# Performance work log

Measured on AMD Instinct MI355X. Metric: run time of the kernel, lower is better.

## Reference

```python
import jax, jax.numpy as jnp
import numpy as np
from jax import lax

# Production-scale dims: batch, seq_len, tag_size (incl. START/STOP tags)
B, S, T = 512, 512, 64


def setup_inputs() -> dict:
    key = jax.random.key(0)
    k1, k2, k3, k4 = jax.random.split(key, 4)
    feats = jax.random.normal(k1, (B, S, T), dtype=jnp.float32)
    # prefix-contiguous mask (module assumes mask[:, 0] == 1 and length-style masks)
    lengths = jax.random.randint(k2, (B,), S // 2, S + 1)
    mask = jnp.arange(S)[None, :] < lengths[:, None]  # (B, S) bool
    tags = jax.random.randint(k3, (B, S), 0, T - 2)  # gold tags exclude START/STOP
    transitions = jax.random.normal(k4, (T, T), dtype=jnp.float32) * 0.1
    return {"feats": feats, "mask": mask, "tags": tags, "transitions": transitions}


def _crf_nll(feats, transitions, mask, tags):
    b, s, t = feats.shape
    START, STOP = t - 2, t - 1  # START_TAG = -2, STOP_TAG = -1

    # ---- forward (log partition), matches _calculate_PZ ----
    # partition init: scores[0][:, START, :] = feats[:,0,:] + transitions[START, :]
    init = feats[:, 0, :] + transitions[START][None, :]  # (b, t)

    feats_t = jnp.swapaxes(feats, 0, 1)  # (s, b, t)
    mask_t = jnp.swapaxes(mask, 0, 1)    # (s, b)

    def step(partition, inp):
        f_t, m_t = inp  # (b, t), (b,)
        # cur_values[b, from, to] = feats_t[b, to] + transitions[from, to] + partition[b, from]
        cur = partition[:, :, None] + transitions[None, :, :] + f_t[:, None, :]
        new_p = jax.nn.logsumexp(cur, axis=1)  # reduce over 'from' -> (b, t)
        partition = jnp.where(m_t[:, None], new_p, partition)
        return partition, None

    partition, _ = lax.scan(step, init, (feats_t[1:], mask_t[1:]))

    # final transition to STOP
    final = jax.nn.logsumexp(partition[:, :, None] + transitions[None, :, :], axis=1)
    forward_score = final[:, STOP].sum()

    # ---- gold score, matches _score_sentence ----
    prev = jnp.concatenate(
        [jnp.full((b, 1), START, dtype=tags.dtype), tags[:, :-1]], axis=1
    )  # (b, s): previous tag, START at position 0
    emit = jnp.take_along_axis(feats, tags[:, :, None], axis=2)[:, :, 0]  # (b, s)
    tg_energy = emit + transitions[prev, tags]  # (b, s)
    gold = jnp.where(mask, tg_energy, jnp.zeros((), feats.dtype)).sum()
    lengths = mask.sum(axis=1).astype(jnp.int32)  # (b,)
    end_ids = jnp.take_along_axis(tags, (lengths - 1)[:, None].astype(tags.dtype), axis=1)[:, 0]
    gold = gold + transitions[end_ids, STOP].sum()

    # average_batch = False
    return forward_score - gold


def reference(feats, mask, tags, transitions):
    return _crf_nll(feats, transitions, mask, tags)
```

## Files before the change

### kernel.cpp

```cpp
#include <hip/hip_runtime.h>

#define BB 512
#define SS 512
#define TT 64
#define START_TAG 62
#define STOP_TAG 63

#define LOG2E 1.4426950408889634f
#define LN2   0.6931471805599453f

typedef _Float16 h2 __attribute__((ext_vector_type(2)));
typedef _Float16 h8 __attribute__((ext_vector_type(8)));
typedef float    f4 __attribute__((ext_vector_type(4)));

__device__ __forceinline__ h2 pkrtz(float a, float b) {
    return __builtin_bit_cast(h2, __builtin_amdgcn_cvt_pkrtz(a, b));
}

__global__ void __launch_bounds__(128)
__attribute__((amdgpu_waves_per_eu(1, 1))) crf_main(
    const float* __restrict__ feats, const int* __restrict__ mask,
    const int* __restrict__ tags, const float* __restrict__ trans,
    float* __restrict__ out)
{
    const int b    = blockIdx.x;
    const int tid  = threadIdx.x;
    const int lane = tid & 63;

    const float* frow = feats + (size_t)b * SS * TT;
    const int*   mrow = mask + b * SS;

    __shared__ __align__(16) _Float16 febuf[8][TT];

    if (tid < 64) {
        const int g  = lane >> 4;
        const int cg = lane & 15;

        int cnt = 0;
        #pragma unroll
        for (int s = lane; s < SS; s += 64) cnt += (mrow[s] != 0);
        #pragma unroll
        for (int off = 32; off; off >>= 1) cnt += __shfl_xor(cnt, off);
        const int len = cnt;

        const int to_base   = 16 * (cg >> 2) + (cg & 3);
        const int from_base = 16 * g;
        h8 A[4][2];
        #pragma unroll
        for (int tt = 0; tt < 4; ++tt)
            #pragma unroll
            for (int kc = 0; kc < 2; ++kc)
                #pragma unroll
                for (int j = 0; j < 8; ++j)
                    A[tt][kc][j] = (_Float16)__builtin_amdgcn_exp2f(
                        trans[(from_base + 8 * kc + j) * TT
                              + (to_base + 4 * tt)] * LOG2E);

        const float offs = frow[0] + trans[START_TAG * TT + 0];
        h8 B0, B1;
        #pragma unroll
        for (int sl = 0; sl < 8; ++sl) {
            const int t0 = 16 * g + sl, t1 = t0 + 8;
            B0[sl] = (_Float16)__builtin_amdgcn_exp2f(
                (frow[t0] + trans[START_TAG * TT + t0] - offs) * LOG2E);
            B1[sl] = (_Float16)__builtin_amdgcn_exp2f(
                (frow[t1] + trans[START_TAG * TT + t1] - offs) * LOG2E);
        }
        int ksum = 0;
        const f4 Z = {0.f, 0.f, 0.f, 0.f};

        float fr[8];
        #pragma unroll
        for (int j = 0; j < 8; ++j) {
            int r = 1 + j; if (r > SS - 1) r = SS - 1;
            fr[j] = frow[(size_t)r * TT + lane];
        }
        #pragma unroll
        for (int j = 0; j < 4; ++j)
            febuf[(1 + j) & 7][lane] =
                (_Float16)__builtin_amdgcn_exp2f(fr[j] * LOG2E);

        auto step = [&](int row) {
            const _Float16* fb = &febuf[row & 7][16 * g];
            const h8 fe0 = *(const h8*)(fb);
            const h8 fe1 = *(const h8*)(fb + 8);
            f4 d0 = __builtin_amdgcn_mfma_f32_16x16x32_f16(A[0][0], B0, Z, 0, 0, 0);
            f4 d1 = __builtin_amdgcn_mfma_f32_16x16x32_f16(A[1][0], B0, Z, 0, 0, 0);
            f4 d2 = __builtin_amdgcn_mfma_f32_16x16x32_f16(A[2][0], B0, Z, 0, 0, 0);
            f4 d3 = __builtin_amdgcn_mfma_f32_16x16x32_f16(A[3][0], B0, Z, 0, 0, 0);
            d0 = __builtin_amdgcn_mfma_f32_16x16x32_f16(A[0][1], B1, d0, 0, 0, 0);
            d1 = __builtin_amdgcn_mfma_f32_16x16x32_f16(A[1][1], B1, d1, 0, 0, 0);
            d2 = __builtin_amdgcn_mfma_f32_16x16x32_f16(A[2][1], B1, d2, 0, 0, 0);
            d3 = __builtin_amdgcn_mfma_f32_16x16x32_f16(A[3][1], B1, d3, 0, 0, 0);
            const int eb = (__builtin_amdgcn_readfirstlane(
                                __float_as_int(d0[0])) >> 23) & 0xff;
            ksum += eb - 127;
            const float sc = __int_as_float((254 - eb) << 23);
            const h2 p0 = pkrtz(d0[0] * sc, d0[1] * sc);
            const h2 p1 = pkrtz(d0[2] * sc, d0[3] * sc);
            const h2 p2 = pkrtz(d1[0] * sc, d1[1] * sc);
            const h2 p3 = pkrtz(d1[2] * sc, d1[3] * sc);
            const h2 p4 = pkrtz(d2[0] * sc, d2[1] * sc);
            const h2 p5 = pkrtz(d2[2] * sc, d2[3] * sc);
            const h2 p6 = pkrtz(d3[0] * sc, d3[1] * sc);
            const h2 p7 = pkrtz(d3[2] * sc, d3[3] * sc);
            const h2 q0 = p0 * __builtin_shufflevector(fe0, fe0, 0, 1);
            const h2 q1 = p1 * __builtin_shufflevector(fe0, fe0, 2, 3);
            const h2 q2 = p2 * __builtin_shufflevector(fe0, fe0, 4, 5);
            const h2 q3 = p3 * __builtin_shufflevector(fe0, fe0, 6, 7);
            const h2 q4 = p4 * __builtin_shufflevector(fe1, fe1, 0, 1);
            const h2 q5 = p5 * __builtin_shufflevector(fe1, fe1, 2, 3);
            const h2 q6 = p6 * __builtin_shufflevector(fe1, fe1, 4, 5);
            const h2 q7 = p7 * __builtin_shufflevector(fe1, fe1, 6, 7);
            B0 = __builtin_shufflevector(
                     __builtin_shufflevector(q0, q1, 0, 1, 2, 3),
                     __builtin_shufflevector(q2, q3, 0, 1, 2, 3),
                     0, 1, 2, 3, 4, 5, 6, 7);
            B1 = __builtin_shufflevector(
                     __builtin_shufflevector(q4, q5, 0, 1, 2, 3),
                     __builtin_shufflevector(q6, q7, 0, 1, 2, 3),
                     0, 1, 2, 3, 4, 5, 6, 7);
        };

        int s = 1;
        for (; s + 3 < len; s += 4) {
            float n0, n1, n2, n3;
            {
                int r0 = s + 8, r1 = s + 9, r2 = s + 10, r3 = s + 11;
                if (r0 > SS - 1) r0 = SS - 1;
                if (r1 > SS - 1) r1 = SS - 1;
                if (r2 > SS - 1) r2 = SS - 1;
                if (r3 > SS - 1) r3 = SS - 1;
                n0 = frow[(size_t)r0 * TT + lane];
                n1 = frow[(size_t)r1 * TT + lane];
                n2 = frow[(size_t)r2 * TT + lane];
                n3 = frow[(size_t)r3 * TT + lane];
            }
            febuf[(s + 4) & 7][lane] =
                (_Float16)__builtin_amdgcn_exp2f(fr[4] * LOG2E);
            febuf[(s + 5) & 7][lane] =
                (_Float16)__builtin_amdgcn_exp2f(fr[5] * LOG2E);
            febuf[(s + 6) & 7][lane] =
                (_Float16)__builtin_amdgcn_exp2f(fr[6] * LOG2E);
            febuf[(s + 7) & 7][lane] =
                (_Float16)__builtin_amdgcn_exp2f(fr[7] * LOG2E);

            step(s); step(s + 1); step(s + 2); step(s + 3);

            #pragma unroll
            for (int j = 0; j < 4; ++j) fr[j] = fr[j + 4];
            fr[4] = n0; fr[5] = n1; fr[6] = n2; fr[7] = n3;
        }

        const int rem = len - s;
        if (rem > 0) step(s);
        if (rem > 1) step(s + 1);
        if (rem > 2) step(s + 2);

        float e = 0.f;
        #pragma unroll
        for (int sl = 0; sl < 8; ++sl) {
            const int t0 = 16 * g + sl, t1 = t0 + 8;
            e += (float)B0[sl] * __builtin_amdgcn_exp2f(
                     trans[t0 * TT + STOP_TAG] * LOG2E);
            e += (float)B1[sl] * __builtin_amdgcn_exp2f(
                     trans[t1 * TT + STOP_TAG] * LOG2E);
        }
        e += __shfl_xor(e, 16);
        e += __shfl_xor(e, 32);

        if (lane == 0)
            atomicAdd(out, offs + (float)ksum * LN2
                           + LN2 * __builtin_amdgcn_logf(e));
    } else {
        const int* trow = tags + b * SS;
        int   cnt = 0;
        float acc = 0.f;
        for (int s = lane; s < SS; s += 64) {
            if (mrow[s] != 0) {
                ++cnt;
                const int tag  = trow[s];
                const int prev = (s == 0) ? START_TAG : trow[s - 1];
                acc += frow[(size_t)s * TT + tag] + trans[prev * TT + tag];
            }
        }
        #pragma unroll
        for (int off = 32; off; off >>= 1) {
            acc += __shfl_xor(acc, off);
            cnt += __shfl_xor(cnt, off);
        }
        if (lane == 0) {
            const int end_id = trow[cnt - 1];
            atomicAdd(out, -(acc + trans[end_id * TT + STOP_TAG]));
        }
    }
}

extern "C" void kernel_launch(void* const* d_in, const int* in_sizes, int n_in,
                              void* d_out, int out_size, void* d_ws, size_t ws_size,
                              hipStream_t stream) {
    const float* feats = (const float*)d_in[0];
    const int*   mask  = (const int*)d_in[1];
    const int*   tags  = (const int*)d_in[2];
    const float* trans = (const float*)d_in[3];
    float* out = (float*)d_out;

    (void)hipMemsetAsync(out, 0, sizeof(float), stream);
    crf_main<<<BB, 128, 0, stream>>>(feats, mask, tags, trans, out);
}
```

Baseline: 186.4 us.

## Split CRF forward recurrence into forward and backward halves on two waves

```diff
diff --git a/kernel.cpp b/kernel.cpp
--- a/kernel.cpp
+++ b/kernel.cpp
@@ -16,82 +16,120 @@
 __device__ __forceinline__ h2 pkrtz(float a, float b) {
     return __builtin_bit_cast(h2, __builtin_amdgcn_cvt_pkrtz(a, b));
 }
-
-__global__ void __launch_bounds__(128)
-__attribute__((amdgpu_waves_per_eu(1, 1))) crf_main(
+__device__ __forceinline__ f4 MF(h8 a, h8 b, f4 c) {
+    return __builtin_amdgcn_mfma_f32_16x16x32_f16(a, b, c, 0, 0, 0);
+}
+
+__global__ void __launch_bounds__(192) crf_main(
     const float* __restrict__ feats, const int* __restrict__ mask,
     const int* __restrict__ tags, const float* __restrict__ trans,
     float* __restrict__ out)
 {
     const int b    = blockIdx.x;
     const int tid  = threadIdx.x;
+    const int wv   = tid >> 6;
     const int lane = tid & 63;
 
     const float* frow = feats + (size_t)b * SS * TT;
     const int*   mrow = mask + b * SS;
 
-    __shared__ __align__(16) _Float16 febuf[8][TT];
-
-    if (tid < 64) {
+    __shared__ __align__(16) _Float16 febuf[2][8][TT];
+    __shared__ __align__(16) float xbuf[TT];
+    __shared__ __align__(16) float ybuf[TT];
+    __shared__ int ks_sh[2];
+
+    int cnt = 0;
+    #pragma unroll
+    for (int s = lane; s < SS; s += 64) cnt += (mrow[s] != 0);
+    #pragma unroll
+    for (int off = 32; off; off >>= 1) cnt += __shfl_xor(cnt, off);
+    const int len = cnt;
+    const int h   = len >> 1;
+
+    float offs = 0.f;
+    int   ksum = 0;
+
+    if (wv < 2) {
+        const bool isF = (wv == 0);
         const int g  = lane >> 4;
         const int cg = lane & 15;
-
-        int cnt = 0;
-        #pragma unroll
-        for (int s = lane; s < SS; s += 64) cnt += (mrow[s] != 0);
-        #pragma unroll
-        for (int off = 32; off; off >>= 1) cnt += __shfl_xor(cnt, off);
-        const int len = cnt;
-
         const int to_base   = 16 * (cg >> 2) + (cg & 3);
-        const int from_base = 16 * g;
+        const int nstep = isF ? h : (len - 1 - h);
+        const int r0    = isF ? 0 : (len - 1);
+        const int dir   = isF ? 1 : -1;
+        _Float16 (*febw)[TT] = febuf[wv];
+
         h8 A[4][2];
         #pragma unroll
         for (int tt = 0; tt < 4; ++tt)
             #pragma unroll
             for (int kc = 0; kc < 2; ++kc)
                 #pragma unroll
-                for (int j = 0; j < 8; ++j)
-                    A[tt][kc][j] = (_Float16)__builtin_amdgcn_exp2f(
-                        trans[(from_base + 8 * kc + j) * TT
-                              + (to_base + 4 * tt)] * LOG2E);
-
-        const float offs = frow[0] + trans[START_TAG * TT + 0];
+                for (int j = 0; j < 8; ++j) {
+                    const int kt = 16 * g + 8 * kc + j;
+                    const int ot = to_base + 4 * tt;
+                    const int ix = isF ? (kt * TT + ot) : (ot * TT + kt);
+                    A[tt][kc][j] =
+                        (_Float16)__builtin_amdgcn_exp2f(trans[ix] * LOG2E);
+                }
+
         h8 B0, B1;
-        #pragma unroll
-        for (int sl = 0; sl < 8; ++sl) {
-            const int t0 = 16 * g + sl, t1 = t0 + 8;
-            B0[sl] = (_Float16)__builtin_amdgcn_exp2f(
-                (frow[t0] + trans[START_TAG * TT + t0] - offs) * LOG2E);
-            B1[sl] = (_Float16)__builtin_amdgcn_exp2f(
-                (frow[t1] + trans[START_TAG * TT + t1] - offs) * LOG2E);
-        }
-        int ksum = 0;
+        if (isF) {
+            offs = frow[0] + trans[START_TAG * TT + 0];
+            #pragma unroll
+            for (int sl = 0; sl < 8; ++sl) {
+                const int t0 = 16 * g + sl, t1 = t0 + 8;
+                B0[sl] = (_Float16)__builtin_amdgcn_exp2f(
+                    (trans[START_TAG * TT + t0] - offs) * LOG2E);
+                B1[sl] = (_Float16)__builtin_amdgcn_exp2f(
+                    (trans[START_TAG * TT + t1] - offs) * LOG2E);
+            }
+        } else {
+            #pragma unroll
+            for (int sl = 0; sl < 8; ++sl) {
+                const int t0 = 16 * g + sl, t1 = t0 + 8;
+                B0[sl] = (_Float16)__builtin_amdgcn_exp2f(
+                    trans[t0 * TT + STOP_TAG] * LOG2E);
+                B1[sl] = (_Float16)__builtin_amdgcn_exp2f(
+                    trans[t1 * TT + STOP_TAG] * LOG2E);
+            }
+        }
+
+        auto rowOf = [&](int idx) {
+            int r = r0 + dir * idx;
+            return r < 0 ? 0 : (r > SS - 1 ? SS - 1 : r);
+        };
+
+        float fr[8];
+        #pragma unroll
+        for (int j = 0; j < 8; ++j)
+            fr[j] = frow[(size_t)rowOf(j) * TT + lane];
+        #pragma unroll
+        for (int j = 0; j < 4; ++j)
+            febw[rowOf(j) & 7][lane] =
+                (_Float16)__builtin_amdgcn_exp2f(fr[j] * LOG2E);
+        h8 cL0, cL1, cL2, cL3, cH0, cH1, cH2, cH3;
+        {
+            const _Float16* p0 = &febw[rowOf(0) & 7][16 * g];
+            const _Float16* p1 = &febw[rowOf(1) & 7][16 * g];
+            const _Float16* p2 = &febw[rowOf(2) & 7][16 * g];
+            const _Float16* p3 = &febw[rowOf(3) & 7][16 * g];
+            cL0 = *(const h8*)p0; cH0 = *(const h8*)(p0 + 8);
+            cL1 = *(const h8*)p1; cH1 = *(const h8*)(p1 + 8);
+            cL2 = *(const h8*)p2; cH2 = *(const h8*)(p2 + 8);
+            cL3 = *(const h8*)p3; cH3 = *(const h8*)(p3 + 8);
+        }
+
         const f4 Z = {0.f, 0.f, 0.f, 0.f};
-
-        float fr[8];
-        #pragma unroll
-        for (int j = 0; j < 8; ++j) {
-            int r = 1 + j; if (r > SS - 1) r = SS - 1;
-            fr[j] = frow[(size_t)r * TT + lane];
-        }
-        #pragma unroll
-        for (int j = 0; j < 4; ++j)
-            febuf[(1 + j) & 7][lane] =
-                (_Float16)__builtin_amdgcn_exp2f(fr[j] * LOG2E);
-
-        auto step = [&](int row) {
-            const _Float16* fb = &febuf[row & 7][16 * g];
-            const h8 fe0 = *(const h8*)(fb);
-            const h8 fe1 = *(const h8*)(fb + 8);
-            f4 d0 = __builtin_amdgcn_mfma_f32_16x16x32_f16(A[0][0], B0, Z, 0, 0, 0);
-            f4 d1 = __builtin_amdgcn_mfma_f32_16x16x32_f16(A[1][0], B0, Z, 0, 0, 0);
-            f4 d2 = __builtin_amdgcn_mfma_f32_16x16x32_f16(A[2][0], B0, Z, 0, 0, 0);
-            f4 d3 = __builtin_amdgcn_mfma_f32_16x16x32_f16(A[3][0], B0, Z, 0, 0, 0);
-            d0 = __builtin_amdgcn_mfma_f32_16x16x32_f16(A[0][1], B1, d0, 0, 0, 0);
-            d1 = __builtin_amdgcn_mfma_f32_16x16x32_f16(A[1][1], B1, d1, 0, 0, 0);
-            d2 = __builtin_amdgcn_mfma_f32_16x16x32_f16(A[2][1], B1, d2, 0, 0, 0);
-            d3 = __builtin_amdgcn_mfma_f32_16x16x32_f16(A[3][1], B1, d3, 0, 0, 0);
+        auto STEP = [&](h8 feL, h8 feH) {
+            const h8 a00 = A[0][0] * feL, a01 = A[0][1] * feH;
+            const h8 a10 = A[1][0] * feL, a11 = A[1][1] * feH;
+            const h8 a20 = A[2][0] * feL, a21 = A[2][1] * feH;
+            const h8 a30 = A[3][0] * feL, a31 = A[3][1] * feH;
+            const f4 d0 = MF(a01, B1, MF(a00, B0, Z));
+            const f4 d1 = MF(a11, B1, MF(a10, B0, Z));
+            const f4 d2 = MF(a21, B1, MF(a20, B0, Z));
+            const f4 d3 = MF(a31, B1, MF(a30, B0, Z));
             const int eb = (__builtin_amdgcn_readfirstlane(
                                 __float_as_int(d0[0])) >> 23) & 0xff;
             ksum += eb - 127;
@@ -104,95 +142,92 @@
             const h2 p5 = pkrtz(d2[2] * sc, d2[3] * sc);
             const h2 p6 = pkrtz(d3[0] * sc, d3[1] * sc);
             const h2 p7 = pkrtz(d3[2] * sc, d3[3] * sc);
-            const h2 q0 = p0 * __builtin_shufflevector(fe0, fe0, 0, 1);
-            const h2 q1 = p1 * __builtin_shufflevector(fe0, fe0, 2, 3);
-            const h2 q2 = p2 * __builtin_shufflevector(fe0, fe0, 4, 5);
-            const h2 q3 = p3 * __builtin_shufflevector(fe0, fe0, 6, 7);
-            const h2 q4 = p4 * __builtin_shufflevector(fe1, fe1, 0, 1);
-            const h2 q5 = p5 * __builtin_shufflevector(fe1, fe1, 2, 3);
-            const h2 q6 = p6 * __builtin_shufflevector(fe1, fe1, 4, 5);
-            const h2 q7 = p7 * __builtin_shufflevector(fe1, fe1, 6, 7);
             B0 = __builtin_shufflevector(
-                     __builtin_shufflevector(q0, q1, 0, 1, 2, 3),
-                     __builtin_shufflevector(q2, q3, 0, 1, 2, 3),
+                     __builtin_shufflevector(p0, p1, 0, 1, 2, 3),
+                     __builtin_shufflevector(p2, p3, 0, 1, 2, 3),
                      0, 1, 2, 3, 4, 5, 6, 7);
             B1 = __builtin_shufflevector(
-                     __builtin_shufflevector(q4, q5, 0, 1, 2, 3),
-                     __builtin_shufflevector(q6, q7, 0, 1, 2, 3),
+                     __builtin_shufflevector(p4, p5, 0, 1, 2, 3),
+                     __builtin_shufflevector(p6, p7, 0, 1, 2, 3),
                      0, 1, 2, 3, 4, 5, 6, 7);
         };
 
-        int s = 1;
-        for (; s + 3 < len; s += 4) {
-            float n0, n1, n2, n3;
-            {
-                int r0 = s + 8, r1 = s + 9, r2 = s + 10, r3 = s + 11;
-                if (r0 > SS - 1) r0 = SS - 1;
-                if (r1 > SS - 1) r1 = SS - 1;
-                if (r2 > SS - 1) r2 = SS - 1;
-                if (r3 > SS - 1) r3 = SS - 1;
-                n0 = frow[(size_t)r0 * TT + lane];
-                n1 = frow[(size_t)r1 * TT + lane];
-                n2 = frow[(size_t)r2 * TT + lane];
-                n3 = frow[(size_t)r3 * TT + lane];
-            }
-            febuf[(s + 4) & 7][lane] =
+        int i = 0;
+        for (; i + 3 < nstep; i += 4) {
+            const float n0 = frow[(size_t)rowOf(i + 8)  * TT + lane];
+            const float n1 = frow[(size_t)rowOf(i + 9)  * TT + lane];
+            const float n2 = frow[(size_t)rowOf(i + 10) * TT + lane];
+            const float n3 = frow[(size_t)rowOf(i + 11) * TT + lane];
+            febw[rowOf(i + 4) & 7][lane] =
                 (_Float16)__builtin_amdgcn_exp2f(fr[4] * LOG2E);
-            febuf[(s + 5) & 7][lane] =
+            febw[rowOf(i + 5) & 7][lane] =
                 (_Float16)__builtin_amdgcn_exp2f(fr[5] * LOG2E);
-            febuf[(s + 6) & 7][lane] =
+            febw[rowOf(i + 6) & 7][lane] =
                 (_Float16)__builtin_amdgcn_exp2f(fr[6] * LOG2E);
-            febuf[(s + 7) & 7][lane] =
+            febw[rowOf(i + 7) & 7][lane] =
                 (_Float16)__builtin_amdgcn_exp2f(fr[7] * LOG2E);
-
-            step(s); step(s + 1); step(s + 2); step(s + 3);
-
+            const _Float16* q0 = &febw[rowOf(i + 4) & 7][16 * g];
+            const _Float16* q1 = &febw[rowOf(i + 5) & 7][16 * g];
+            const _Float16* q2 = &febw[rowOf(i + 6) & 7][16 * g];
+            const _Float16* q3 = &febw[rowOf(i + 7) & 7][16 * g];
+            const h8 nL0 = *(const h8*)q0, nH0 = *(const h8*)(q0 + 8);
+            const h8 nL1 = *(const h8*)q1, nH1 = *(const h8*)(q1 + 8);
+            const h8 nL2 = *(const h8*)q2, nH2 = *(const h8*)(q2 + 8);
+            const h8 nL3 = *(const h8*)q3, nH3 = *(const h8*)(q3 + 8);
+
+            STEP(cL0, cH0); STEP(cL1, cH1); STEP(cL2, cH2); STEP(cL3, cH3);
+
+            cL0 = nL0; cH0 = nH0; cL1 = nL1; cH1 = nH1;
+            cL2 = nL2; cH2 = nH2; cL3 = nL3; cH3 = nH3;
             #pragma unroll
             for (int j = 0; j < 4; ++j) fr[j] = fr[j + 4];
             fr[4] = n0; fr[5] = n1; fr[6] = n2; fr[7] = n3;
         }
 
-        const int rem = len - s;
-        if (rem > 0) step(s);
-        if (rem > 1) step(s + 1);
-        if (rem > 2) step(s + 2);
-
-        float e = 0.f;
-        #pragma unroll
-        for (int sl = 0; sl < 8; ++sl) {
-            const int t0 = 16 * g + sl, t1 = t0 + 8;
-            e += (float)B0[sl] * __builtin_amdgcn_exp2f(
-                     trans[t0 * TT + STOP_TAG] * LOG2E);
-            e += (float)B1[sl] * __builtin_amdgcn_exp2f(
-                     trans[t1 * TT + STOP_TAG] * LOG2E);
-        }
-        e += __shfl_xor(e, 16);
-        e += __shfl_xor(e, 32);
-
-        if (lane == 0)
-            atomicAdd(out, offs + (float)ksum * LN2
-                           + LN2 * __builtin_amdgcn_logf(e));
+        const int rem = nstep - i;
+        if (rem > 0) STEP(cL0, cH0);
+        if (rem > 1) STEP(cL1, cH1);
+        if (rem > 2) STEP(cL2, cH2);
+
+        float* obuf = isF ? xbuf : ybuf;
+        if (cg == 0) {
+            #pragma unroll
+            for (int sl = 0; sl < 8; ++sl) {
+                obuf[16 * g + sl]     = (float)B0[sl];
+                obuf[16 * g + 8 + sl] = (float)B1[sl];
+            }
+        }
+        if (lane == 0) ks_sh[wv] = ksum;
     } else {
         const int* trow = tags + b * SS;
-        int   cnt = 0;
-        float acc = 0.f;
+        int   gcnt = 0;
+        float acc  = 0.f;
         for (int s = lane; s < SS; s += 64) {
             if (mrow[s] != 0) {
-                ++cnt;
+                ++gcnt;
                 const int tag  = trow[s];
                 const int prev = (s == 0) ? START_TAG : trow[s - 1];
                 acc += frow[(size_t)s * TT + tag] + trans[prev * TT + tag];
             }
         }
         #pragma unroll
-        for (int off = 32; off; off >>= 1) {
-            acc += __shfl_xor(acc, off);
-            cnt += __shfl_xor(cnt, off);
-        }
+        for (int off = 32; off; off >>= 1) acc += __shfl_xor(acc, off);
         if (lane == 0) {
-            const int end_id = trow[cnt - 1];
+            const int end_id = trow[len - 1];
             atomicAdd(out, -(acc + trans[end_id * TT + STOP_TAG]));
         }
+    }
+
+    __syncthreads();
+
+    if (wv == 0) {
+        float z = xbuf[lane] * ybuf[lane] *
+                  __builtin_amdgcn_exp2f(frow[(size_t)h * TT + lane] * LOG2E);
+        #pragma unroll
+        for (int off = 32; off; off >>= 1) z += __shfl_xor(z, off);
+        if (lane == 0)
+            atomicAdd(out, offs + (float)(ksum + ks_sh[1]) * LN2
+                           + LN2 * __builtin_amdgcn_logf(z));
     }
 }
 
@@ -206,5 +241,5 @@
     float* out = (float*)d_out;
 
     (void)hipMemsetAsync(out, 0, sizeof(float), stream);
-    crf_main<<<BB, 128, 0, stream>>>(feats, mask, tags, trans, out);
-}
+    crf_main<<<BB, 192, 0, stream>>>(feats, mask, tags, trans, out);
+}
```

After: 186.0 us. About the same (-0.2%).
